# Optimization experiments

Measured on AMD Instinct MI355X. Metric: run time of the kernel, lower is better.

## Reference

```python
import jax, jax.numpy as jnp
import numpy as np


def setup_inputs() -> dict:
    key = jax.random.key(0)
    k1, k2 = jax.random.split(key)
    n, B = 64, 256
    return {
        "out_matrix": jax.random.normal(k1, (n, n, B), dtype=jnp.float32),
        "label_matrix": jax.random.normal(k2, (n, n, B), dtype=jnp.float32),
        "margin": jnp.ones((), dtype=jnp.float32),
        "sample_num": 64,
    }


def reference(out_matrix, label_matrix, margin, sample_num):
    # out_matrix, label_matrix: [n, n, B]; sample_num == n (rows fully used).
    out = jnp.transpose(out_matrix, (2, 0, 1))   # [B, n, n]
    lab = jnp.transpose(label_matrix, (2, 0, 1))  # [B, n, n]
    # Per batch slice, per row r: pairwise diffs d[j,k] = out[r,j]-out[r,k]
    d = out[..., :, None] - out[..., None, :]     # [B, n, n, n]
    l = lab[..., :, None] - lab[..., None, :]     # [B, n, n, n]
    # Hinge: relu(margin - d*l), summed over everything (diagonal contributes margin,
    # matching the original which includes j==k terms).
    loss = jnp.sum(jax.nn.relu(margin - d * l))
    # flat_accuracy per batch slice: argmax over dim 1 of the [n,n] slice,
    # i.e. axis=2 of the [B,n,n] layout (torch argmax(preds,1) on squeezed slice).
    correction_num = jnp.sum(jnp.argmax(out, axis=2) == jnp.argmax(lab, axis=2))
    return loss, correction_num
```

## Files before the change

kernel.cpp:

```cpp
#include <hip/hip_runtime.h>
#include <math.h>


constexpr int N = 64;
constexpr int B = 256;
constexpr int BCHUNK = 64;
constexpr int NJG = 8;
constexpr int JI = 8;
constexpr int THREADS = BCHUNK * NJG;
constexpr int NBLK = N * (B / BCHUNK);

__global__ __launch_bounds__(THREADS)
void pm_hinge_partial(const float* __restrict__ outm,
                      const float* __restrict__ labm,
                      const float* __restrict__ margin,
                      float* __restrict__ ws)
{
    __shared__ __align__(16) float2 s[N * BCHUNK];
    __shared__ float wsum[NJG];

    const int r   = blockIdx.x;
    const int b0  = blockIdx.y * BCHUNK;
    const int t   = threadIdx.x;
    const int blk = blockIdx.y * N + r;

    const float* src_o = outm + (size_t)r * (N * B) + b0;
    const float* src_l = labm + (size_t)r * (N * B) + b0;
#pragma unroll
    for (int f = t; f < (N * BCHUNK) / 4; f += THREADS) {
        const int j  = f >> 4;
        const int b4 = (f & 15) * 4;
        const float4 o4 = *(const float4*)(src_o + j * B + b4);
        const float4 l4 = *(const float4*)(src_l + j * B + b4);
        float4* dst = (float4*)(&s[j * BCHUNK + b4]);
        dst[0] = make_float4(o4.x, l4.x, o4.y, l4.y);
        dst[1] = make_float4(o4.z, l4.z, o4.w, l4.w);
    }
    __syncthreads();

    const float m  = margin[0];
    const int   b  = t & 63;
    const int   jg = t >> 6;

    float oj[JI], lj[JI];
#pragma unroll
    for (int i = 0; i < JI; ++i) {
        const float2 v = s[(jg + NJG * i) * BCHUNK + b];
        oj[i] = v.x; lj[i] = v.y;
    }

    float acc0 = 0.0f, acc1 = 0.0f;
#pragma unroll
    for (int mr = 0; mr < 8; ++mr) {
        const int kbeg = jg + 8 * mr + 1;
        const int kend = (mr == 7) ? N : (jg + 8 * mr + 9);
#pragma unroll 4
        for (int k = kbeg; k < kend; ++k) {
            const float2 v = s[k * BCHUNK + b];
            const float ok = v.x, lk = v.y;
#pragma unroll
            for (int i = 0; i <= mr; ++i) {
                const float tv = fmaxf(fmaf(ok - oj[i], lj[i] - lk, m), 0.0f);
                if (i & 1) acc1 += tv; else acc0 += tv;
            }
        }
    }
    float acc = acc0 + acc1;

    float cnt = 0.0f;
    if (t < 64) {
        const float2 v0 = s[t];
        float bo = v0.x; int io = 0;
        float bl = v0.y; int il = 0;
#pragma unroll 4
        for (int j = 1; j < N; ++j) {
            const float2 v = s[j * BCHUNK + t];
            if (v.x > bo) { bo = v.x; io = j; }
            if (v.y > bl) { bl = v.y; il = j; }
        }
        const unsigned long long mask = __ballot(io == il);
        cnt = (float)__popcll(mask);
    }

#pragma unroll
    for (int off = 32; off > 0; off >>= 1)
        acc += __shfl_down(acc, off, 64);
    if (b == 0) wsum[jg] = acc;
    __syncthreads();
    if (t == 0) {
        float ssum = 0.0f;
#pragma unroll
        for (int w = 0; w < NJG; ++w) ssum += wsum[w];
        ws[blk] = ssum;
        ws[NBLK + blk] = cnt;
    }
}

__global__ __launch_bounds__(64)
void pm_hinge_reduce(const float* __restrict__ ws,
                     const float* __restrict__ margin,
                     float* __restrict__ dout)
{
    const int t = threadIdx.x;
    float s = 0.0f, c = 0.0f;
#pragma unroll
    for (int i = 0; i < NBLK / 64; ++i) {
        s += ws[t + 64 * i];
        c += ws[NBLK + t + 64 * i];
    }
#pragma unroll
    for (int off = 32; off > 0; off >>= 1) {
        s += __shfl_down(s, off, 64);
        c += __shfl_down(c, off, 64);
    }
    if (t == 0) {
        const float m = margin[0];
        dout[0] = 2.0f * s + (float)(N * (size_t)N * B) * fmaxf(m, 0.0f);
        dout[1] = c;
    }
}

extern "C" void kernel_launch(void* const* d_in, const int* in_sizes, int n_in,
                              void* d_out, int out_size, void* d_ws, size_t ws_size,
                              hipStream_t stream) {
    const float* outm   = (const float*)d_in[0];
    const float* labm   = (const float*)d_in[1];
    const float* margin = (const float*)d_in[2];
    float* out = (float*)d_out;
    float* ws  = (float*)d_ws;

    pm_hinge_partial<<<dim3(N, B / BCHUNK), THREADS, 0, stream>>>(outm, labm, margin, ws);
    pm_hinge_reduce<<<1, 64, 0, stream>>>(ws, margin, out);
}
```

Baseline: 69.63 us.

## Fuse final reduction via cooperative grid sync and parallelize argmax across warps

Merges the separate reduce kernel into the main kernel using a cooperative launch and grid-wide sync, so the second kernel launch goes away. It also splits the per-column argmax across all eight waves, each scanning eight rows and writing candidates to shared memory, which wave 0 then merges; previously wave 0 alone scanned all 64 rows. The trade-off is cooperative-launch overhead and a grid barrier across 256 blocks of 512 threads, which requires all blocks to be co-resident.

```diff
diff --git a/kernel.cpp b/kernel.cpp
--- a/kernel.cpp
+++ b/kernel.cpp
@@ -1,5 +1,8 @@
 #include <hip/hip_runtime.h>
+#include <hip/hip_cooperative_groups.h>
 #include <math.h>
+
+namespace cg = cooperative_groups;
 
 
 constexpr int N = 64;
@@ -11,12 +14,14 @@
 constexpr int NBLK = N * (B / BCHUNK);
 
 __global__ __launch_bounds__(THREADS)
-void pm_hinge_partial(const float* __restrict__ outm,
-                      const float* __restrict__ labm,
-                      const float* __restrict__ margin,
-                      float* __restrict__ ws)
+void pm_hinge_fused(const float* __restrict__ outm,
+                    const float* __restrict__ labm,
+                    const float* __restrict__ margin,
+                    float* __restrict__ ws,
+                    float* __restrict__ dout)
 {
     __shared__ __align__(16) float2 s[N * BCHUNK];
+    __shared__ __align__(16) float4 cand[NJG * 64];
     __shared__ float wsum[NJG];
 
     const int r   = blockIdx.x;
@@ -49,6 +54,21 @@
         oj[i] = v.x; lj[i] = v.y;
     }
 
+    {
+        const int jbase = jg * 8;
+        float2 v = s[jbase * BCHUNK + b];
+        float bo = v.x; int io = jbase;
+        float bl = v.y; int il = jbase;
+#pragma unroll
+        for (int jj = 1; jj < 8; ++jj) {
+            v = s[(jbase + jj) * BCHUNK + b];
+            if (v.x > bo) { bo = v.x; io = jbase + jj; }
+            if (v.y > bl) { bl = v.y; il = jbase + jj; }
+        }
+        cand[jg * 64 + b] = make_float4(bo, __int_as_float(io),
+                                        bl, __int_as_float(il));
+    }
+
     float acc0 = 0.0f, acc1 = 0.0f;
 #pragma unroll
     for (int mr = 0; mr < 8; ++mr) {
@@ -67,56 +87,51 @@
     }
     float acc = acc0 + acc1;
 
-    float cnt = 0.0f;
-    if (t < 64) {
-        const float2 v0 = s[t];
-        float bo = v0.x; int io = 0;
-        float bl = v0.y; int il = 0;
-#pragma unroll 4
-        for (int j = 1; j < N; ++j) {
-            const float2 v = s[j * BCHUNK + t];
-            if (v.x > bo) { bo = v.x; io = j; }
-            if (v.y > bl) { bl = v.y; il = j; }
-        }
-        const unsigned long long mask = __ballot(io == il);
-        cnt = (float)__popcll(mask);
-    }
-
 #pragma unroll
     for (int off = 32; off > 0; off >>= 1)
         acc += __shfl_down(acc, off, 64);
     if (b == 0) wsum[jg] = acc;
     __syncthreads();
-    if (t == 0) {
-        float ssum = 0.0f;
+
+    if (t < 64) {
+        float4 c0 = cand[t];
+        float bo = c0.x; int io = __float_as_int(c0.y);
+        float bl = c0.z; int il = __float_as_int(c0.w);
 #pragma unroll
-        for (int w = 0; w < NJG; ++w) ssum += wsum[w];
-        ws[blk] = ssum;
-        ws[NBLK + blk] = cnt;
+        for (int w = 1; w < NJG; ++w) {
+            const float4 cw = cand[w * 64 + t];
+            if (cw.x > bo) { bo = cw.x; io = __float_as_int(cw.y); }
+            if (cw.z > bl) { bl = cw.z; il = __float_as_int(cw.w); }
+        }
+        const unsigned long long mask = __ballot(io == il);
+        if (t == 0) {
+            float ssum = 0.0f;
+#pragma unroll
+            for (int w = 0; w < NJG; ++w) ssum += wsum[w];
+            ws[blk] = ssum;
+            ws[NBLK + blk] = (float)__popcll(mask);
+            __threadfence();
+        }
     }
-}
 
-__global__ __launch_bounds__(64)
-void pm_hinge_reduce(const float* __restrict__ ws,
-                     const float* __restrict__ margin,
-                     float* __restrict__ dout)
-{
-    const int t = threadIdx.x;
-    float s = 0.0f, c = 0.0f;
+    cg::this_grid().sync();
+
+    if (blockIdx.x == 0 && blockIdx.y == 0 && t < 64) {
+        float ssum = 0.0f, c = 0.0f;
 #pragma unroll
-    for (int i = 0; i < NBLK / 64; ++i) {
-        s += ws[t + 64 * i];
-        c += ws[NBLK + t + 64 * i];
-    }
+        for (int i = 0; i < NBLK / 64; ++i) {
+            ssum += ws[t + 64 * i];
+            c    += ws[NBLK + t + 64 * i];
+        }
 #pragma unroll
-    for (int off = 32; off > 0; off >>= 1) {
-        s += __shfl_down(s, off, 64);
-        c += __shfl_down(c, off, 64);
-    }
-    if (t == 0) {
-        const float m = margin[0];
-        dout[0] = 2.0f * s + (float)(N * (size_t)N * B) * fmaxf(m, 0.0f);
-        dout[1] = c;
+        for (int off = 32; off > 0; off >>= 1) {
+            ssum += __shfl_down(ssum, off, 64);
+            c    += __shfl_down(c, off, 64);
+        }
+        if (t == 0) {
+            dout[0] = 2.0f * ssum + (float)(N * (size_t)N * B) * fmaxf(m, 0.0f);
+            dout[1] = c;
+        }
     }
 }
 
@@ -129,6 +144,9 @@
     float* out = (float*)d_out;
     float* ws  = (float*)d_ws;
 
-    pm_hinge_partial<<<dim3(N, B / BCHUNK), THREADS, 0, stream>>>(outm, labm, margin, ws);
-    pm_hinge_reduce<<<1, 64, 0, stream>>>(ws, margin, out);
+    void* args[] = { (void*)&outm, (void*)&labm, (void*)&margin,
+                     (void*)&ws, (void*)&out };
+    hipLaunchCooperativeKernel((const void*)pm_hinge_fused,
+                               dim3(N, B / BCHUNK), dim3(THREADS),
+                               args, 0, stream);
 }
```

New measurement: 111.3 us. +59.9%, slower.
